# Performance work log

Hardware: AMD Instinct MI355X
Metric: run time of the kernel (lower is better)

The kernel has to match this reference:

```python
import jax, jax.numpy as jnp
import numpy as np

B, D, L = 8, 512, 2000          # batch, encoder_out_dim, seq_len
E = 300                          # embedding_dim
N1, N2 = 118, 8929               # hierarchy level sizes


def setup_inputs() -> dict:
    key = jax.random.key(0)
    k = jax.random.split(key, 6)
    H = jax.random.normal(k[0], (B, D, L), dtype=jnp.float32)
    Q1w = jax.random.normal(k[1], (N1, E), dtype=jnp.float32) * 0.05   # cat_embedding_matrix
    Q2w = jax.random.normal(k[2], (N2, E), dtype=jnp.float32) * 0.05   # label_embedding_matrix
    # Q12: xavier_uniform over [N2, N1]
    bound = float(np.sqrt(6.0 / (N1 + N2)))
    Q12w = jax.random.uniform(k[3], (N2, N1), minval=-bound, maxval=bound, dtype=jnp.float32)
    # 1x1 conv mapping: weight [D, E], bias [D] (kernel_size=1 squeezed)
    cbound = float(np.sqrt(1.0 / E))
    Wmap = jax.random.uniform(k[4], (D, E), minval=-cbound, maxval=cbound, dtype=jnp.float32)
    bmap = jax.random.uniform(k[5], (D,), minval=-cbound, maxval=cbound, dtype=jnp.float32)
    return {"H": H, "Q1w": Q1w, "Q2w": Q2w, "Q12w": Q12w, "Wmap": Wmap, "bmap": bmap}


def reference(H, Q1w, Q2w, Q12w, Wmap, bmap):
    # 1x1 conv mapping == affine map over embedding dim: [n, E] @ [E, D] + b
    Q1 = Q1w @ Wmap.T + bmap                      # [N1, D]
    E1 = jnp.einsum('nd,bdl->bnl', Q1, H)         # level-1 scores [B, N1, L]
    A1 = jax.nn.softmax(E1, axis=2)
    C1 = jnp.einsum('bnl,bdl->bnd', A1, H)        # [B, N1, D]
    C1 = jnp.einsum('mn,bnd->bmd', Q12w, C1)      # project to level 2: [B, N2, D]
    Q2 = (Q2w @ Wmap.T + bmap) * C1               # [N2, D] * [B, N2, D]
    E2 = jnp.einsum('bmd,bdl->bml', Q2, H)        # level-2 scores [B, N2, L]
    A2 = jax.nn.softmax(E2, axis=2)
    C2 = jnp.einsum('bml,bdl->bmd', A2, H)        # [B, N2, D]
    return (C2, A2)
```

## Files before the change

kernel.cpp:

```cpp
#include <hip/hip_runtime.h>

typedef short    bf16x8 __attribute__((ext_vector_type(8)));
typedef float    f32x4  __attribute__((ext_vector_type(4)));
typedef unsigned short u16x8 __attribute__((ext_vector_type(8)));

__device__ __forceinline__ unsigned short f2bf(float f) {
    unsigned u = __float_as_uint(f);
    return (unsigned short)((u + 0x7fffu + ((u >> 16) & 1u)) >> 16);
}
__device__ __forceinline__ float bf2f(unsigned short h) {
    return __uint_as_float((unsigned)h << 16);
}

template<bool> struct otype            { using T = float; };
template<>     struct otype<true>      { using T = unsigned short; };

template<int BM,int BN,int TM,int TN,bool BT,bool VA,bool VB,bool OB>
__launch_bounds__(256)
__global__ void gemm_f32(const float* __restrict__ A, int lda, long long sA,
                         const float* __restrict__ B, int ldb, long long sB,
                         void* __restrict__ Cv, int ldc, long long sC,
                         int M, int N, int K,
                         const float* __restrict__ bias,
                         const float* __restrict__ mul, int mulld)
{
    constexpr int BK  = 16;
    constexpr int GSA = BM*4/TM;
    constexpr int GSB = BN*4/TN;
    __shared__ float As[BK][BM+4];
    __shared__ float Bs[BK][BN+4];

    const int bz = blockIdx.z;
    A += (long long)bz * sA;
    B += (long long)bz * sB;
    using OT = typename otype<OB>::T;
    OT* C = (OT*)Cv + (long long)bz * sC;
    const int m0 = blockIdx.y * BM;
    const int n0 = blockIdx.x * BN;
    const int tid = threadIdx.x;
    const int tm = tid >> 4;
    const int tn = tid & 15;

    float acc[TM][TN];
#pragma unroll
    for (int i=0;i<TM;++i)
#pragma unroll
        for (int j=0;j<TN;++j) acc[i][j]=0.f;

    for (int k0=0;k0<K;k0+=BK) {
        if constexpr (VA) {
#pragma unroll
            for (int r=0;r<BM*BK/1024;++r) {
                int v = tid + r*256;
                int m = v >> 2, k4 = (v & 3)*4;
                int gm = m0+m, gk = k0+k4;
                float4 val = make_float4(0.f,0.f,0.f,0.f);
                if (gm < M) {
                    if (gk+3 < K) {
                        val = *reinterpret_cast<const float4*>(A + (long long)gm*lda + gk);
                    } else {
                        float t0 = (gk   < K) ? A[(long long)gm*lda+gk  ] : 0.f;
                        float t1 = (gk+1 < K) ? A[(long long)gm*lda+gk+1] : 0.f;
                        float t2 = (gk+2 < K) ? A[(long long)gm*lda+gk+2] : 0.f;
                        val = make_float4(t0,t1,t2,0.f);
                    }
                }
                As[k4+0][m]=val.x; As[k4+1][m]=val.y; As[k4+2][m]=val.z; As[k4+3][m]=val.w;
            }
        } else {
#pragma unroll
            for (int r=0;r<BM*BK/256;++r) {
                int e = tid + r*256;
                int m = e >> 4, k = e & 15;
                int gm=m0+m, gk=k0+k;
                As[k][m] = (gm<M && gk<K) ? A[(long long)gm*lda+gk] : 0.f;
            }
        }
        if constexpr (!BT) {
            if constexpr (VB) {
#pragma unroll
                for (int r=0;r<BK*BN/1024;++r) {
                    int v = tid + r*256;
                    int k = v / (BN/4), n4 = (v % (BN/4))*4;
                    int gk=k0+k, gn=n0+n4;
                    float4 val = make_float4(0.f,0.f,0.f,0.f);
                    if (gk < K) {
                        if (gn+3 < N) {
                            val = *reinterpret_cast<const float4*>(B + (long long)gk*ldb + gn);
                        } else {
                            float t0=(gn  <N)?B[(long long)gk*ldb+gn  ]:0.f;
                            float t1=(gn+1<N)?B[(long long)gk*ldb+gn+1]:0.f;
                            float t2=(gn+2<N)?B[(long long)gk*ldb+gn+2]:0.f;
                            val = make_float4(t0,t1,t2,0.f);
                        }
                    }
                    Bs[k][n4+0]=val.x; Bs[k][n4+1]=val.y; Bs[k][n4+2]=val.z; Bs[k][n4+3]=val.w;
                }
            } else {
#pragma unroll
                for (int r=0;r<BK*BN/256;++r) {
                    int e = tid + r*256;
                    int k = e / BN, n = e % BN;
                    int gk=k0+k, gn=n0+n;
                    Bs[k][n] = (gk<K && gn<N) ? B[(long long)gk*ldb+gn] : 0.f;
                }
            }
        } else {
            if constexpr (VB) {
#pragma unroll
                for (int r=0;r<BN*BK/1024;++r) {
                    int v = tid + r*256;
                    int n = v >> 2, k4 = (v&3)*4;
                    int gn=n0+n, gk=k0+k4;
                    float4 val = make_float4(0.f,0.f,0.f,0.f);
                    if (gn < N) {
                        if (gk+3 < K) {
                            val = *reinterpret_cast<const float4*>(B + (long long)gn*ldb + gk);
                        } else {
                            float t0=(gk  <K)?B[(long long)gn*ldb+gk  ]:0.f;
                            float t1=(gk+1<K)?B[(long long)gn*ldb+gk+1]:0.f;
                            float t2=(gk+2<K)?B[(long long)gn*ldb+gk+2]:0.f;
                            val=make_float4(t0,t1,t2,0.f);
                        }
                    }
                    Bs[k4+0][n]=val.x; Bs[k4+1][n]=val.y; Bs[k4+2][n]=val.z; Bs[k4+3][n]=val.w;
                }
            } else {
#pragma unroll
                for (int r=0;r<BN*BK/256;++r) {
                    int e = tid + r*256;
                    int n = e >> 4, k = e & 15;
                    int gn=n0+n, gk=k0+k;
                    Bs[k][n] = (gn<N && gk<K) ? B[(long long)gn*ldb+gk] : 0.f;
                }
            }
        }
        __syncthreads();
#pragma unroll
        for (int kk=0;kk<BK;++kk) {
            float a[TM], bb[TN];
#pragma unroll
            for (int g=0;g<TM/4;++g) {
                float4 t = *reinterpret_cast<const float4*>(&As[kk][g*GSA + tm*4]);
                a[4*g+0]=t.x; a[4*g+1]=t.y; a[4*g+2]=t.z; a[4*g+3]=t.w;
            }
#pragma unroll
            for (int g=0;g<TN/4;++g) {
                float4 t = *reinterpret_cast<const float4*>(&Bs[kk][g*GSB + tn*4]);
                bb[4*g+0]=t.x; bb[4*g+1]=t.y; bb[4*g+2]=t.z; bb[4*g+3]=t.w;
            }
#pragma unroll
            for (int i=0;i<TM;++i)
#pragma unroll
                for (int j=0;j<TN;++j)
                    acc[i][j] = fmaf(a[i], bb[j], acc[i][j]);
        }
        __syncthreads();
    }
#pragma unroll
    for (int i=0;i<TM;++i) {
        int row = m0 + (i>>2)*GSA + tm*4 + (i&3);
        if (row < M) {
#pragma unroll
            for (int j=0;j<TN;++j) {
                int col = n0 + (j>>2)*GSB + tn*4 + (j&3);
                if (col < N) {
                    float val = acc[i][j];
                    if (bias) val += bias[col];
                    if (mul)  val *= mul[(long long)row*mulld + col];
                    if constexpr (OB) C[(long long)row*ldc + col] = f2bf(val);
                    else              C[(long long)row*ldc + col] = val;
                }
            }
        }
    }
}

template<unsigned F>
__launch_bounds__(512, 4)
__global__ void gemm_mfma_p(const unsigned short* __restrict__ A, int lda, long long sA,
                            const unsigned short* __restrict__ Bt, int ldb, long long sB,
                            void* __restrict__ Cv, int ldc, long long sC,
                            int M, int Ncols, int NX, int NY, int NT,
                            const float* __restrict__ bias,
                            const float* __restrict__ mul, int ldm,
                            float* __restrict__ partial, long long pstride,
                            const float* __restrict__ hsum,
                            const float* __restrict__ invs,
                            float* __restrict__ a2out,
                            float* __restrict__ dump)
{
    __shared__ unsigned short lds[3][12288];

    const int nwg = gridDim.x;
    const int q = nwg >> 3, r = nwg & 7;
    const int xcd = blockIdx.x & 7, idx = blockIdx.x >> 3;
    const int wg = (xcd < r ? xcd*(q+1) : r*(q+1) + (xcd-r)*q) + idx;
    const int nx = wg % NX;
    const int t1 = wg / NX;
    const int my = t1 % NY;
    const int bz = t1 / NY;

    const int tid  = threadIdx.x;
    const int lane = tid & 63, wid = tid >> 6;
    const int wr = wid >> 2, wc = wid & 3;
    const int fr = lane & 15, fq = lane >> 4;
    const int m0 = my * 128;
    const int n0 = nx * 256;

    A  += (long long)bz * sA;
    Bt += (long long)bz * sB;

    const int srow = tid >> 2;
    const int scz  = (tid & 3) ^ ((srow >> 1) & 3);
    long long arow = m0 + srow; if (arow > M-1) arow = M-1;
    const unsigned short* aSrc  = A  + arow*lda + scz*8;
    const unsigned short* bSrc0 = Bt + (long long)(n0 + srow)*ldb + scz*8;
    const unsigned short* bSrc1 = bSrc0 + 128ll*ldb;

    bool wrblk = false, a2ok = false;
    float invv = 0.f;
    float* a2p = nullptr;
    if constexpr ((F & 64) != 0) {
        wrblk = (nx == 0);
        if (wrblk) {
            const int rrow = m0 + srow;
            a2ok = rrow < M;
            const long long ridx = (long long)bz*M + (a2ok ? rrow : M-1);
            invv = invs[ridx];
            asm volatile("" : "+v"(invv));
            a2p = a2out + ridx*2000ll;
        }
    }

    int aoff[4], boff[4];
#pragma unroll
    for (int m=0;m<4;++m) {
        const int ra = wr*64 + m*16 + fr;
        aoff[m] = ra*64 + ((fq ^ ((ra>>1)&3))*16);
    }
#pragma unroll
    for (int n=0;n<4;++n) {
        const int rb = wc*64 + n*16 + fr;
        boff[n] = 8192 + rb*64 + ((fq ^ ((rb>>1)&3))*16);
    }

    f32x4 acc[4][4];
#pragma unroll
    for (int i=0;i<4;++i)
#pragma unroll
        for (int j=0;j<4;++j) acc[i][j] = (f32x4)(0.f);

    auto stage = [&](int s, int t) {
        const int koff = t*32;
        char* base = (char*)&lds[s][0];
        __builtin_amdgcn_global_load_lds(
            (const __attribute__((address_space(1))) void*)(aSrc + koff),
            (__attribute__((address_space(3))) void*)(base + tid*16), 16, 0, 0);
        __builtin_amdgcn_global_load_lds(
            (const __attribute__((address_space(1))) void*)(bSrc0 + koff),
            (__attribute__((address_space(3))) void*)(base + 8192 + tid*16), 16, 0, 0);
        __builtin_amdgcn_global_load_lds(
            (const __attribute__((address_space(1))) void*)(bSrc1 + koff),
            (__attribute__((address_space(3))) void*)(base + 16384 + tid*16), 16, 0, 0);
    };

    stage(0, 0);
    stage(1, NT > 1 ? 1 : 0);
    asm volatile("s_waitcnt vmcnt(3)" ::: "memory");
    __builtin_amdgcn_s_barrier();

    int cur = 0, stg = 2;
    for (int kt = 0; kt < NT; ++kt) {
        int tnx = kt + 2; if (tnx > NT-1) tnx = NT-1;
        stage(stg, tnx);
        const char* bp = (const char*)&lds[cur][0];
        bf16x8 a[4], b[4];
#pragma unroll
        for (int m=0;m<4;++m) a[m] = *(const bf16x8*)(bp + aoff[m]);
#pragma unroll
        for (int n=0;n<4;++n) b[n] = *(const bf16x8*)(bp + boff[n]);
        __builtin_amdgcn_s_setprio(1);
#pragma unroll
        for (int m=0;m<4;++m)
#pragma unroll
            for (int n=0;n<4;++n)
                acc[m][n] = __builtin_amdgcn_mfma_f32_16x16x32_bf16(a[m], b[n], acc[m][n], 0, 0, 0);
        __builtin_amdgcn_s_setprio(0);
        if constexpr ((F & 64) != 0) {
            if (wrblk) {
                u16x8 av = *(const u16x8*)(bp + (tid << 4));
                const int col0 = kt*32 + scz*8;
                const bool ok = a2ok && (col0 < 2000);
                float* p0 = ok ? (a2p + col0) : (dump + (tid << 3));
                float4 o0, o1;
                o0.x = fmaf(bf2f((unsigned short)av[0]), invv, invv);
                o0.y = fmaf(bf2f((unsigned short)av[1]), invv, invv);
                o0.z = fmaf(bf2f((unsigned short)av[2]), invv, invv);
                o0.w = fmaf(bf2f((unsigned short)av[3]), invv, invv);
                o1.x = fmaf(bf2f((unsigned short)av[4]), invv, invv);
                o1.y = fmaf(bf2f((unsigned short)av[5]), invv, invv);
                o1.z = fmaf(bf2f((unsigned short)av[6]), invv, invv);
                o1.w = fmaf(bf2f((unsigned short)av[7]), invv, invv);
                *(float4*)(p0    ) = o0;
                *(float4*)(p0 + 4) = o1;
            }
        }
        asm volatile("s_waitcnt lgkmcnt(0)" ::: "memory");
        if constexpr ((F & 64) != 0) {
            if (wrblk) asm volatile("s_waitcnt vmcnt(5)" ::: "memory");
            else       asm volatile("s_waitcnt vmcnt(3)" ::: "memory");
        } else {
            asm volatile("s_waitcnt vmcnt(3)" ::: "memory");
        }
        __builtin_amdgcn_s_barrier();
        cur = (cur == 2) ? 0 : cur + 1;
        stg = (stg == 2) ? 0 : stg + 1;
    }

    if constexpr ((F & 16) != 0) {
        __shared__ float sp[4][128];
        unsigned short* Cb = (unsigned short*)Cv + (long long)bz * sC;
        float rp[4][4];
#pragma unroll
        for (int m=0;m<4;++m)
#pragma unroll
            for (int j=0;j<4;++j) rp[m][j] = 0.f;
#pragma unroll
        for (int m=0;m<4;++m) {
            const int rb = m0 + wr*64 + m*16 + fq*4;
#pragma unroll
            for (int n=0;n<4;++n) {
                const int col = n0 + wc*64 + n*16 + fr;
#pragma unroll
                for (int j=0;j<4;++j) {
                    float x = __expf(acc[m][n][j]) - 1.0f;
                    rp[m][j] += x;
                    const int row = rb + j;
                    if (row < M) Cb[(long long)row*ldc + col] = f2bf(x);
                }
            }
        }
#pragma unroll
        for (int m=0;m<4;++m)
#pragma unroll
            for (int j=0;j<4;++j) {
                float s = rp[m][j];
                s += __shfl_xor(s, 1); s += __shfl_xor(s, 2);
                s += __shfl_xor(s, 4); s += __shfl_xor(s, 8);
                rp[m][j] = s;
            }
        if (fr == 0) {
#pragma unroll
            for (int m=0;m<4;++m)
#pragma unroll
                for (int j=0;j<4;++j)
                    sp[wc][wr*64 + m*16 + fq*4 + j] = rp[m][j];
        }
        __syncthreads();
        if (tid < 128) {
            const int row = m0 + tid;
            if (row < M) {
                float s = sp[0][tid] + sp[1][tid] + sp[2][tid] + sp[3][tid];
                partial[(long long)nx*pstride + (long long)bz*M + row] = s;
            }
        }
    } else if constexpr ((F & 8) != 0) {
        unsigned short* Ct = (unsigned short*)Cv + (long long)bz * sC;
#pragma unroll
        for (int m=0;m<4;++m) {
            const int rb = m0 + wr*64 + m*16 + fq*4;
#pragma unroll
            for (int n=0;n<4;++n) {
                const int col = n0 + wc*64 + n*16 + fr;
                if (col < Ncols) {
#pragma unroll
                    for (int j=0;j<4;++j) {
                        const int row = rb + j;
                        float val = (row < M) ? acc[m][n][j] : 0.f;
                        Ct[(long long)col*ldc + row] = f2bf(val);
                    }
                }
            }
        }
    } else {
        float*          Cf = (float*)Cv + (long long)bz * sC;
        unsigned short* Cb = (unsigned short*)Cv + (long long)bz * sC;
#pragma unroll
        for (int m=0;m<4;++m) {
            const int rb = m0 + wr*64 + m*16 + fq*4;
#pragma unroll
            for (int n=0;n<4;++n) {
                const int col = n0 + wc*64 + n*16 + fr;
                if (col < Ncols) {
                    float bv = 0.f, hv = 0.f;
                    if constexpr ((F & 1) != 0) bv = bias[col];
                    if constexpr ((F & 32) != 0) hv = hsum[(long long)bz*Ncols + col];
#pragma unroll
                    for (int j=0;j<4;++j) {
                        const int row = rb + j;
                        if (row < M) {
                            float val = acc[m][n][j];
                            if constexpr ((F & 1) != 0)  val += bv;
                            if constexpr ((F & 2) != 0)  val *= mul[(long long)row*ldm + col];
                            if constexpr ((F & 32) != 0) val = (val + hv) * invs[(long long)bz*M + row];
                            if constexpr ((F & 4) != 0)  Cb[(long long)row*ldc + col] = f2bf(val);
                            else                         Cf[(long long)row*ldc + col] = val;
                        }
                    }
                }
            }
        }
    }
}

template<bool AF32>
__launch_bounds__(512, 2)
__global__ void gemm_mfma(const void* __restrict__ Ain, int lda, long long sA,
                          const unsigned short* __restrict__ Bt, int ldb, long long sB,
                          float* __restrict__ C, int ldc, long long sC,
                          int M, int N, int K, int NT)
{
    __shared__ unsigned short As[2][128*32];
    __shared__ unsigned short Bs[2][256*32];

    const int tid  = threadIdx.x;
    const int lane = tid & 63, wid = tid >> 6;
    const int wr = wid >> 2, wc = wid & 3;
    const int fr = lane & 15, fq = lane >> 4;
    const int bz = blockIdx.z;
    const int m0 = blockIdx.y * 128;
    const int n0 = blockIdx.x * 256;

    const unsigned short* Ab = nullptr;
    const float*          Af = nullptr;
    if constexpr (AF32) Af = (const float*)Ain + (long long)bz * sA;
    else                Ab = (const unsigned short*)Ain + (long long)bz * sA;
    Bt += (long long)bz * sB;
    C  += (long long)bz * sC;

    const int srow = tid >> 2;
    const int sc   = tid & 3;
    const int scz  = sc ^ ((srow >> 1) & 3);
    int arow = m0 + srow; if (arow > M-1) arow = M-1;
    const bool am_ok = (m0 + srow) < M;
    const long long brow0 = n0 + srow;
    const long long brow1 = n0 + 128 + srow;
    const int ldsA  = wid << 10;
    const int ldsB0 = wid << 10;
    const int ldsB1 = 8192 + (wid << 10);

    f32x4 acc[4][4];
#pragma unroll
    for (int i=0;i<4;++i)
#pragma unroll
        for (int j=0;j<4;++j) acc[i][j] = (f32x4)(0.f);

    auto stage = [&](int buf, int t) {
        const long long koff = (long long)t * 32;
        __builtin_amdgcn_global_load_lds(
            (const __attribute__((address_space(1))) void*)(Bt + brow0*ldb + koff + scz*8),
            (__attribute__((address_space(3))) void*)((char*)&Bs[buf][0] + ldsB0), 16, 0, 0);
        __builtin_amdgcn_global_load_lds(
            (const __attribute__((address_space(1))) void*)(Bt + brow1*ldb + koff + scz*8),
            (__attribute__((address_space(3))) void*)((char*)&Bs[buf][0] + ldsB1), 16, 0, 0);
        if constexpr (!AF32) {
            __builtin_amdgcn_global_load_lds(
                (const __attribute__((address_space(1))) void*)(Ab + (long long)arow*lda + koff + scz*8),
                (__attribute__((address_space(3))) void*)((char*)&As[buf][0] + ldsA), 16, 0, 0);
        } else {
            const float* src = Af + (long long)arow*lda + koff + scz*8;
            const int kk = t*32 + scz*8;
            float4 z = make_float4(0.f,0.f,0.f,0.f);
            float4 v0 = (am_ok && kk   < K) ? *(const float4*)(src  ) : z;
            float4 v1 = (am_ok && kk+4 < K) ? *(const float4*)(src+4) : z;
            u16x8 o;
            o[0]=f2bf(v0.x); o[1]=f2bf(v0.y); o[2]=f2bf(v0.z); o[3]=f2bf(v0.w);
            o[4]=f2bf(v1.x); o[5]=f2bf(v1.y); o[6]=f2bf(v1.z); o[7]=f2bf(v1.w);
            *(u16x8*)((char*)&As[buf][0] + tid*16) = o;
        }
    };

    stage(0, 0);
    int cur = 0;
    for (int t = 0; t < NT; ++t) {
        __syncthreads();
        if (t + 1 < NT) stage(cur ^ 1, t + 1);
        const unsigned short* as = As[cur];
        const unsigned short* bs = Bs[cur];
        bf16x8 a[4], b[4];
#pragma unroll
        for (int m=0;m<4;++m) {
            const int ra = wr*64 + m*16 + fr;
            a[m] = *(const bf16x8*)(as + ra*32 + (fq ^ ((ra>>1)&3))*8);
        }
#pragma unroll
        for (int n=0;n<4;++n) {
            const int rb = wc*64 + n*16 + fr;
            b[n] = *(const bf16x8*)(bs + rb*32 + (fq ^ ((rb>>1)&3))*8);
        }
        __builtin_amdgcn_s_setprio(1);
#pragma unroll
        for (int m=0;m<4;++m)
#pragma unroll
            for (int n=0;n<4;++n)
                acc[m][n] = __builtin_amdgcn_mfma_f32_16x16x32_bf16(a[m], b[n], acc[m][n], 0, 0, 0);
        __builtin_amdgcn_s_setprio(0);
        cur ^= 1;
    }
#pragma unroll
    for (int m=0;m<4;++m) {
        const int rb = m0 + wr*64 + m*16 + fq*4;
#pragma unroll
        for (int n=0;n<4;++n) {
            const int col = n0 + wc*64 + n*16 + fr;
            if (col < N) {
#pragma unroll
                for (int j=0;j<4;++j) {
                    const int row = rb + j;
                    if (row < M) C[(long long)row*ldc + col] = acc[m][n][j];
                }
            }
        }
    }
}

__global__ __launch_bounds__(256) void prep_h(const float* __restrict__ H,
                                              unsigned short* __restrict__ Hb,
                                              unsigned short* __restrict__ Htb,
                                              float* __restrict__ hpart)
{
    __shared__ unsigned short T[64][80];
    const int bz = blockIdx.z;
    const int d0 = blockIdx.y * 64;
    const int l0 = blockIdx.x * 64;
    const float* Hsrc = H + ((long long)bz*512 + d0) * 2000;
    const int tid = threadIdx.x;
    const int dl = tid >> 2;
    const int lc = (tid & 3) * 16;
    float4 v[4];
    float s = 0.f;
#pragma unroll
    for (int i=0;i<4;++i) {
        const int gl = l0 + lc + i*4;
        v[i] = make_float4(0.f,0.f,0.f,0.f);
        if (gl < 2000) v[i] = *(const float4*)(Hsrc + (long long)dl*2000 + gl);
        s += (v[i].x + v[i].y) + (v[i].z + v[i].w);
        T[lc+i*4+0][dl] = f2bf(v[i].x);
        T[lc+i*4+1][dl] = f2bf(v[i].y);
        T[lc+i*4+2][dl] = f2bf(v[i].z);
        T[lc+i*4+3][dl] = f2bf(v[i].w);
    }
    {
        unsigned short* hb = Hb + ((long long)bz*512 + d0 + dl)*2048 + l0 + lc;
        u16x8 h0, h1;
        h0[0]=f2bf(v[0].x); h0[1]=f2bf(v[0].y); h0[2]=f2bf(v[0].z); h0[3]=f2bf(v[0].w);
        h0[4]=f2bf(v[1].x); h0[5]=f2bf(v[1].y); h0[6]=f2bf(v[1].z); h0[7]=f2bf(v[1].w);
        h1[0]=f2bf(v[2].x); h1[1]=f2bf(v[2].y); h1[2]=f2bf(v[2].z); h1[3]=f2bf(v[2].w);
        h1[4]=f2bf(v[3].x); h1[5]=f2bf(v[3].y); h1[6]=f2bf(v[3].z); h1[7]=f2bf(v[3].w);
        *(u16x8*)(hb    ) = h0;
        *(u16x8*)(hb + 8) = h1;
    }
    s += __shfl_xor(s, 1);
    s += __shfl_xor(s, 2);
    if ((tid & 3) == 0)
        hpart[(long long)blockIdx.x*4096 + bz*512 + d0 + dl] = s;
    __syncthreads();
    unsigned short* Hdst = Htb + ((long long)bz*2048 + l0) * 512 + d0;
    const int ll = tid >> 2;
    const int dc = (tid & 3) * 16;
    u16x8 w0 = *(const u16x8*)&T[ll][dc];
    u16x8 w1 = *(const u16x8*)&T[ll][dc+8];
    *(u16x8*)(Hdst + (long long)ll*512 + dc    ) = w0;
    *(u16x8*)(Hdst + (long long)ll*512 + dc + 8) = w1;
}

__global__ __launch_bounds__(256) void reduce_hsum(const float* __restrict__ hpart,
                                                   float* __restrict__ Hsum)
{
    const int r = blockIdx.x*256 + threadIdx.x;
    float s = 0.f;
#pragma unroll
    for (int i=0;i<32;++i) s += hpart[(long long)i*4096 + r];
    Hsum[r] = s;
}

__global__ __launch_bounds__(256) void invs_k(const float* __restrict__ partial,
                                              long long pstride,
                                              float* __restrict__ invs, int n)
{
    const int r = blockIdx.x*256 + threadIdx.x;
    if (r < n) {
        float s = 0.f;
#pragma unroll
        for (int i=0;i<8;++i) s += partial[i*pstride + r];
        invs[r] = 1.0f / (2000.0f + s);
    }
}

__global__ __launch_bounds__(256) void cvt_pad_bf16(const float* __restrict__ H,
                                                    unsigned short* __restrict__ Hb)
{
    const long long idx = (long long)blockIdx.x * 256 + threadIdx.x;
    const long long row = idx >> 8;
    const int l0 = (int)(idx & 255) * 8;
    u16x8 o = (u16x8)(unsigned short)0;
    if (l0 + 8 <= 2000) {
        const float* s = H + row*2000 + l0;
        float4 v0 = *(const float4*)(s);
        float4 v1 = *(const float4*)(s+4);
        o[0]=f2bf(v0.x); o[1]=f2bf(v0.y); o[2]=f2bf(v0.z); o[3]=f2bf(v0.w);
        o[4]=f2bf(v1.x); o[5]=f2bf(v1.y); o[6]=f2bf(v1.z); o[7]=f2bf(v1.w);
    }
    *(u16x8*)(Hb + row*2048 + l0) = o;
}

__global__ __launch_bounds__(256) void cvt_transpose_bf16(const float* __restrict__ H,
                                                          unsigned short* __restrict__ Ht)
{
    __shared__ unsigned short T[64][80];
    const int bz = blockIdx.z;
    const int d0 = blockIdx.y * 64;
    const int l0 = blockIdx.x * 64;
    const float* Hsrc = H + ((long long)bz*512 + d0) * 2000;
    unsigned short* Hdst = Ht + ((long long)bz*2048 + l0) * 512 + d0;
    const int tid = threadIdx.x;
    const int dl = tid >> 2;
    const int lc = (tid & 3) * 16;
#pragma unroll
    for (int i=0;i<4;++i) {
        const int l = lc + i*4;
        const int gl = l0 + l;
        float4 v = make_float4(0.f,0.f,0.f,0.f);
        if (gl < 2000) v = *(const float4*)(Hsrc + (long long)dl*2000 + gl);
        T[l+0][dl] = f2bf(v.x);
        T[l+1][dl] = f2bf(v.y);
        T[l+2][dl] = f2bf(v.z);
        T[l+3][dl] = f2bf(v.w);
    }
    __syncthreads();
    const int ll = tid >> 2;
    const int dc = (tid & 3) * 16;
    u16x8 w0 = *(const u16x8*)&T[ll][dc];
    u16x8 w1 = *(const u16x8*)&T[ll][dc+8];
    *(u16x8*)(Hdst + (long long)ll*512 + dc    ) = w0;
    *(u16x8*)(Hdst + (long long)ll*512 + dc + 8) = w1;
}

__global__ __launch_bounds__(256) void cvt_rows_bf16(const float* __restrict__ src,
                                                     unsigned short* __restrict__ dst,
                                                     long long rows, int scols, int dcols)
{
    const long long i = (long long)blockIdx.x * 256 + threadIdx.x;
    if (i < rows * (long long)dcols) {
        const long long r = i / dcols;
        const int c = (int)(i - r*dcols);
        dst[i] = (c < scols) ? f2bf(src[r*scols + c]) : (unsigned short)0;
    }
}

__global__ __launch_bounds__(256) void softmax_rows(float* __restrict__ X, int L,
                                                    unsigned short* __restrict__ Xb, int Lb)
{
    const long long row = blockIdx.x;
    float* x = X + row * (long long)L;
    const int tid = threadIdx.x;
    const int nv = L >> 2;
    const bool h0 = tid < nv;
    const bool h1 = tid + 256 < nv;
    float4 t0 = make_float4(0.f,0.f,0.f,0.f);
    float4 t1 = make_float4(0.f,0.f,0.f,0.f);
    float mx = -3.402823e38f;
    if (h0) { t0 = *reinterpret_cast<const float4*>(x + 4*tid);
              mx = fmaxf(fmaxf(t0.x,t0.y), fmaxf(t0.z,t0.w)); }
    if (h1) { t1 = *reinterpret_cast<const float4*>(x + 4*(tid+256));
              mx = fmaxf(mx, fmaxf(fmaxf(t1.x,t1.y), fmaxf(t1.z,t1.w))); }
    __shared__ float sred[4];
#pragma unroll
    for (int o=32;o;o>>=1) mx = fmaxf(mx, __shfl_xor(mx, o));
    if ((tid & 63)==0) sred[tid>>6] = mx;
    __syncthreads();
    mx = fmaxf(fmaxf(sred[0],sred[1]), fmaxf(sred[2],sred[3]));
    __syncthreads();
    float s = 0.f;
    if (h0) {
        t0.x=__expf(t0.x-mx); t0.y=__expf(t0.y-mx); t0.z=__expf(t0.z-mx); t0.w=__expf(t0.w-mx);
        s += (t0.x+t0.y)+(t0.z+t0.w);
    }
    if (h1) {
        t1.x=__expf(t1.x-mx); t1.y=__expf(t1.y-mx); t1.z=__expf(t1.z-mx); t1.w=__expf(t1.w-mx);
        s += (t1.x+t1.y)+(t1.z+t1.w);
    }
#pragma unroll
    for (int o=32;o;o>>=1) s += __shfl_xor(s, o);
    if ((tid & 63)==0) sred[tid>>6] = s;
    __syncthreads();
    s = (sred[0]+sred[1])+(sred[2]+sred[3]);
    const float inv = 1.0f / s;
    if (h0) { t0.x*=inv; t0.y*=inv; t0.z*=inv; t0.w*=inv;
              *reinterpret_cast<float4*>(x + 4*tid) = t0; }
    if (h1) { t1.x*=inv; t1.y*=inv; t1.z*=inv; t1.w*=inv;
              *reinterpret_cast<float4*>(x + 4*(tid+256)) = t1; }
    if (Xb) {
        unsigned short* xb = Xb + row * (long long)Lb;
        if (h0) {
            ushort4 o; o.x=f2bf(t0.x); o.y=f2bf(t0.y); o.z=f2bf(t0.z); o.w=f2bf(t0.w);
            *reinterpret_cast<ushort4*>(xb + 4*tid) = o;
        }
        if (h1) {
            ushort4 o; o.x=f2bf(t1.x); o.y=f2bf(t1.y); o.z=f2bf(t1.z); o.w=f2bf(t1.w);
            *reinterpret_cast<ushort4*>(xb + 4*(tid+256)) = o;
        }
        if (tid < (Lb - L)/4) {
            ushort4 z; z.x=z.y=z.z=z.w=0;
            *reinterpret_cast<ushort4*>(xb + L + 4*tid) = z;
        }
    }
}

extern "C" void kernel_launch(void* const* d_in, const int* in_sizes, int n_in,
                              void* d_out, int out_size, void* d_ws, size_t ws_size,
                              hipStream_t stream)
{
    const float* H    = (const float*)d_in[0];
    const float* Q1w  = (const float*)d_in[1];
    const float* Q2w  = (const float*)d_in[2];
    const float* Q12w = (const float*)d_in[3];
    const float* Wmap = (const float*)d_in[4];
    const float* bmap = (const float*)d_in[5];

    constexpr long long B=8, D=512, L=2000, N1=118, N2=8929;
    constexpr long long C2E = B*N2*D;
    float* out = (float*)d_out;
    float* C2  = out;
    float* A2  = out + C2E;

    dim3 blk(256);

    size_t off = 0;
    auto alloc = [&](size_t n)->size_t { off = (off + 255) & ~(size_t)255; size_t o = off; off += n; return o; };
    const size_t oHb    = alloc(8ll*512*2048*2);
    const size_t oHtb   = alloc(8ll*2048*512*2);
    const size_t oWb    = alloc(512ll*320*2);
    const size_t oQ1wb  = alloc(118ll*320*2);
    const size_t oQ2wb  = alloc(8929ll*320*2);
    const size_t oQ12wb = alloc(8929ll*128*2);
    const size_t oQ1b   = alloc(118ll*512*2);
    const size_t oEmb   = alloc(8929ll*512*4);
    const size_t oE1    = alloc(8ll*118*2000*4);
    const size_t oA1b   = alloc(8ll*118*2048*2);
    const size_t oC1tb  = alloc(8ll*512*128*2);
    const size_t oQ2b   = alloc(8ll*8929*512*2);
    const size_t oA2b   = alloc(8ll*8929*2048*2);
    const size_t oPart  = alloc(8ll*8*8929*4);
    const size_t oInvs  = alloc(8ll*8929*4);
    const size_t oHsum  = alloc(8ll*512*4);
    const size_t oHpart = alloc(32ll*4096*4);
    const size_t FULL_NEED = off;

    char* ws = (char*)d_ws;

    if (ws_size >= FULL_NEED) {
        unsigned short* Hb    = (unsigned short*)(ws + oHb);
        unsigned short* Htb   = (unsigned short*)(ws + oHtb);
        unsigned short* Wb    = (unsigned short*)(ws + oWb);
        unsigned short* Q1wb  = (unsigned short*)(ws + oQ1wb);
        unsigned short* Q2wb  = (unsigned short*)(ws + oQ2wb);
        unsigned short* Q12wb = (unsigned short*)(ws + oQ12wb);
        unsigned short* Q1b   = (unsigned short*)(ws + oQ1b);
        float*          emb   = (float*)(ws + oEmb);
        float*          E1    = (float*)(ws + oE1);
        unsigned short* A1b   = (unsigned short*)(ws + oA1b);
        unsigned short* C1tb  = (unsigned short*)(ws + oC1tb);
        unsigned short* Q2b   = (unsigned short*)(ws + oQ2b);
        unsigned short* A2b   = (unsigned short*)(ws + oA2b);
        float*          part  = (float*)(ws + oPart);
        float*          invs  = (float*)(ws + oInvs);
        float*          Hsum  = (float*)(ws + oHsum);
        float*          hpart = (float*)(ws + oHpart);

        prep_h<<<dim3(32,8,8), blk, 0, stream>>>(H, Hb, Htb, hpart);
        reduce_hsum<<<dim3(16), blk, 0, stream>>>(hpart, Hsum);
        cvt_rows_bf16<<<dim3((512*320+255)/256), blk, 0, stream>>>(Wmap, Wb, 512, 300, 320);
        cvt_rows_bf16<<<dim3((118*320+255)/256), blk, 0, stream>>>(Q1w, Q1wb, 118, 300, 320);
        cvt_rows_bf16<<<dim3((8929*320+255)/256), blk, 0, stream>>>(Q2w, Q2wb, 8929, 300, 320);
        cvt_rows_bf16<<<dim3((8929*128+255)/256), blk, 0, stream>>>(Q12w, Q12wb, 8929, 118, 128);

        gemm_mfma_p<5><<<dim3(2), dim3(512), 0, stream>>>(
            Q1wb, 320, 0, Wb, 320, 0, Q1b, 512, 0, 118, 512, 2, 1, 10,
            bmap, nullptr, 0, nullptr, 0, nullptr, nullptr, nullptr, nullptr);
        gemm_mfma_p<1><<<dim3(140), dim3(512), 0, stream>>>(
            Q2wb, 320, 0, Wb, 320, 0, emb, 512, 0, 8929, 512, 2, 70, 10,
            bmap, nullptr, 0, nullptr, 0, nullptr, nullptr, nullptr, nullptr);
        gemm_mfma_p<0><<<dim3(64), dim3(512), 0, stream>>>(
            Q1b, 512, 0, Htb, 512, 2048*512, E1, 2000, N1*L, 118, 2000, 8, 1, 16,
            nullptr, nullptr, 0, nullptr, 0, nullptr, nullptr, nullptr, nullptr);
        softmax_rows<<<dim3((unsigned)(B*N1)), blk, 0, stream>>>(E1, 2000, A1b, 2048);
        gemm_mfma_p<12><<<dim3(16), dim3(512), 0, stream>>>(
            A1b, 2048, N1*2048, Hb, 2048, 512*2048, C1tb, 128, 512*128, 118, 512, 2, 1, 64,
            nullptr, nullptr, 0, nullptr, 0, nullptr, nullptr, nullptr, nullptr);
        gemm_mfma_p<6><<<dim3(1120), dim3(512), 0, stream>>>(
            Q12wb, 128, 0, C1tb, 128, 512*128, Q2b, 512, N2*D, 8929, 512, 2, 70, 4,
            nullptr, emb, 512, nullptr, 0, nullptr, nullptr, nullptr, nullptr);
        gemm_mfma_p<16><<<dim3(4480), dim3(512), 0, stream>>>(
            Q2b, 512, N2*D, Htb, 512, 2048*512, A2b, 2048, N2*2048, 8929, 2048, 8, 70, 16,
            nullptr, nullptr, 0, part, 8ll*8929, nullptr, nullptr, nullptr, nullptr);
        invs_k<<<dim3(280), blk, 0, stream>>>(part, 8ll*8929, invs, (int)(B*N2));
        gemm_mfma_p<96><<<dim3(1120), dim3(512), 0, stream>>>(
            A2b, 2048, N2*2048, Hb, 2048, 512*2048, C2, 512, N2*D, 8929, 512, 2, 70, 64,
            nullptr, nullptr, 0, nullptr, 0, Hsum, invs, A2, part);
        return;
    }

    float* Q1  = A2;
    float* emb = Q1  + N1*D;
    float* E1  = emb + N2*D;
    float* C1  = E1  + B*N1*L;

    gemm_f32<64,64,4,4,true,true,true,false><<<dim3(8,2,1), blk, 0, stream>>>(
        Q1w, 300, 0, Wmap, 300, 0, Q1, 512, 0, (int)N1, (int)D, 300, bmap, nullptr, 0);
    gemm_f32<64,64,4,4,true,true,true,false><<<dim3(8,140,1), blk, 0, stream>>>(
        Q2w, 300, 0, Wmap, 300, 0, emb, 512, 0, (int)N2, (int)D, 300, bmap, nullptr, 0);
    gemm_f32<64,64,4,4,false,true,true,false><<<dim3(32,2,8), blk, 0, stream>>>(
        Q1, 512, 0, H, 2000, D*L, E1, 2000, N1*L, (int)N1, (int)L, (int)D, nullptr, nullptr, 0);
    softmax_rows<<<dim3((unsigned)(B*N1)), blk, 0, stream>>>(E1, (int)L, nullptr, 0);
    gemm_f32<64,64,4,4,true,true,true,false><<<dim3(8,2,8), blk, 0, stream>>>(
        E1, 2000, N1*L, H, 2000, D*L, C1, 512, N1*D, (int)N1, (int)D, (int)L, nullptr, nullptr, 0);

    constexpr long long HBE = 8ll*512*2048;
    if (ws_size >= (size_t)(2*HBE*sizeof(unsigned short))) {
        unsigned short* Hb  = (unsigned short*)d_ws;
        unsigned short* Htb = Hb + HBE;
        cvt_pad_bf16<<<dim3(4096), blk, 0, stream>>>(H, Hb);
        cvt_transpose_bf16<<<dim3(32,8,8), blk, 0, stream>>>(H, Htb);
        unsigned short* Q2b = (unsigned short*)C2;
        gemm_f32<64,64,4,4,false,false,true,true><<<dim3(8,140,8), blk, 0, stream>>>(
            Q12w, 118, 0, C1, 512, N1*D, Q2b, 512, N2*D, (int)N2, (int)D, (int)N1, nullptr, emb, 512);
        gemm_mfma_p<0><<<dim3(4480), dim3(512), 0, stream>>>(
            Q2b, 512, N2*D, Htb, 512, 2048*512, A2, 2000, N2*L, (int)N2, (int)L, 8, 70, 16,
            nullptr, nullptr, 0, nullptr, 0, nullptr, nullptr, nullptr, nullptr);
        softmax_rows<<<dim3((unsigned)(B*N2)), blk, 0, stream>>>(A2, (int)L, nullptr, 0);
        gemm_mfma<true><<<dim3(2,70,8), dim3(512), 0, stream>>>(
            A2, 2000, N2*L, Hb, 2048, 512*2048, C2, 512, N2*D,
            (int)N2, (int)D, 2000, 63);
    } else {
        float* Q2 = C2;
        gemm_f32<64,64,4,4,false,false,true,false><<<dim3(8,140,8), blk, 0, stream>>>(
            Q12w, 118, 0, C1, 512, N1*D, Q2, 512, N2*D, (int)N2, (int)D, (int)N1, nullptr, emb, 512);
        gemm_f32<128,128,8,8,false,true,true,false><<<dim3(16,70,8), blk, 0, stream>>>(
            Q2, 512, N2*D, H, 2000, D*L, A2, 2000, N2*L, (int)N2, (int)L, (int)D, nullptr, nullptr, 0);
        softmax_rows<<<dim3((unsigned)(B*N2)), blk, 0, stream>>>(A2, (int)L, nullptr, 0);
        gemm_f32<128,128,8,8,true,true,true,false><<<dim3(4,70,8), blk, 0, stream>>>(
            A2, 2000, N2*L, H, 2000, D*L, C2, 512, N2*D, (int)N2, (int)D, (int)L, nullptr, nullptr, 0);
    }
}
```

Measured before the change: 810.4 us.

## Fuse prep kernels, reuse fused-softmax GEMM path for level 1, split A2 writes

Merges the H transpose/convert kernel and four weight-conversion kernels into one launch. The level-1 path drops the fp32 score buffer and separate softmax: it uses the exp-partial-sum GEMM variant (F=16) plus invs_k, and folds normalization into the C1 GEMM epilogue via Hsum and invs1. The embedding intermediate is stored as bf16 and read through a new F&128 multiply path. The fp32 A2 output writes are spread across both column blocks by alternating k-tiles, instead of being done only by the nx==0 blocks. This cuts launches and memory traffic but adds bf16 rounding on the embedding product.

```diff
diff --git a/kernel.cpp b/kernel.cpp
--- a/kernel.cpp
+++ b/kernel.cpp
@@ -218,19 +218,18 @@
     const unsigned short* bSrc0 = Bt + (long long)(n0 + srow)*ldb + scz*8;
     const unsigned short* bSrc1 = bSrc0 + 128ll*ldb;
 
-    bool wrblk = false, a2ok = false;
+    bool a2ok = false;
+    int  par  = 0;
     float invv = 0.f;
     float* a2p = nullptr;
     if constexpr ((F & 64) != 0) {
-        wrblk = (nx == 0);
-        if (wrblk) {
-            const int rrow = m0 + srow;
-            a2ok = rrow < M;
-            const long long ridx = (long long)bz*M + (a2ok ? rrow : M-1);
-            invv = invs[ridx];
-            asm volatile("" : "+v"(invv));
-            a2p = a2out + ridx*2000ll;
-        }
+        par = nx & 1;
+        const int rrow = m0 + srow;
+        a2ok = rrow < M;
+        const long long ridx = (long long)bz*M + (a2ok ? rrow : M-1);
+        invv = invs[ridx];
+        asm volatile("" : "+v"(invv));
+        a2p = a2out + ridx*2000ll;
     }
 
     int aoff[4], boff[4];
@@ -288,7 +287,7 @@
                 acc[m][n] = __builtin_amdgcn_mfma_f32_16x16x32_bf16(a[m], b[n], acc[m][n], 0, 0, 0);
         __builtin_amdgcn_s_setprio(0);
         if constexpr ((F & 64) != 0) {
-            if (wrblk) {
+            if ((kt & 1) == par) {
                 u16x8 av = *(const u16x8*)(bp + (tid << 4));
                 const int col0 = kt*32 + scz*8;
                 const bool ok = a2ok && (col0 < 2000);
@@ -308,8 +307,7 @@
         }
         asm volatile("s_waitcnt lgkmcnt(0)" ::: "memory");
         if constexpr ((F & 64) != 0) {
-            if (wrblk) asm volatile("s_waitcnt vmcnt(5)" ::: "memory");
-            else       asm volatile("s_waitcnt vmcnt(3)" ::: "memory");
+            asm volatile("s_waitcnt vmcnt(5)" ::: "memory");
         } else {
             asm volatile("s_waitcnt vmcnt(3)" ::: "memory");
         }
@@ -374,10 +372,16 @@
             for (int n=0;n<4;++n) {
                 const int col = n0 + wc*64 + n*16 + fr;
                 if (col < Ncols) {
+                    float hv = 0.f;
+                    if constexpr ((F & 32) != 0) hv = hsum[(long long)bz*Ncols + col];
 #pragma unroll
                     for (int j=0;j<4;++j) {
                         const int row = rb + j;
-                        float val = (row < M) ? acc[m][n][j] : 0.f;
+                        float val = 0.f;
+                        if (row < M) {
+                            val = acc[m][n][j];
+                            if constexpr ((F & 32) != 0) val = (val + hv) * invs[(long long)bz*M + row];
+                        }
                         Ct[(long long)col*ldc + row] = f2bf(val);
                     }
                 }
@@ -401,11 +405,12 @@
                         const int row = rb + j;
                         if (row < M) {
                             float val = acc[m][n][j];
-                            if constexpr ((F & 1) != 0)  val += bv;
-                            if constexpr ((F & 2) != 0)  val *= mul[(long long)row*ldm + col];
-                            if constexpr ((F & 32) != 0) val = (val + hv) * invs[(long long)bz*M + row];
-                            if constexpr ((F & 4) != 0)  Cb[(long long)row*ldc + col] = f2bf(val);
-                            else                         Cf[(long long)row*ldc + col] = val;
+                            if constexpr ((F & 1)   != 0) val += bv;
+                            if constexpr ((F & 2)   != 0) val *= mul[(long long)row*ldm + col];
+                            if constexpr ((F & 128) != 0) val *= bf2f(((const unsigned short*)mul)[(long long)row*ldm + col]);
+                            if constexpr ((F & 32)  != 0) val = (val + hv) * invs[(long long)bz*M + row];
+                            if constexpr ((F & 4)   != 0) Cb[(long long)row*ldc + col] = f2bf(val);
+                            else                          Cf[(long long)row*ldc + col] = val;
                         }
                     }
                 }
@@ -525,54 +530,76 @@
     }
 }
 
-__global__ __launch_bounds__(256) void prep_h(const float* __restrict__ H,
-                                              unsigned short* __restrict__ Hb,
-                                              unsigned short* __restrict__ Htb,
-                                              float* __restrict__ hpart)
+__global__ __launch_bounds__(256) void mega_prep(const float* __restrict__ H,
+                                                 unsigned short* __restrict__ Hb,
+                                                 unsigned short* __restrict__ Htb,
+                                                 float* __restrict__ hpart,
+                                                 const float* __restrict__ Wmap,  unsigned short* __restrict__ Wb,
+                                                 const float* __restrict__ Q1w,   unsigned short* __restrict__ Q1wb,
+                                                 const float* __restrict__ Q2w,   unsigned short* __restrict__ Q2wb,
+                                                 const float* __restrict__ Q12w,  unsigned short* __restrict__ Q12wb)
 {
     __shared__ unsigned short T[64][80];
-    const int bz = blockIdx.z;
-    const int d0 = blockIdx.y * 64;
-    const int l0 = blockIdx.x * 64;
-    const float* Hsrc = H + ((long long)bz*512 + d0) * 2000;
     const int tid = threadIdx.x;
-    const int dl = tid >> 2;
-    const int lc = (tid & 3) * 16;
-    float4 v[4];
-    float s = 0.f;
-#pragma unroll
-    for (int i=0;i<4;++i) {
-        const int gl = l0 + lc + i*4;
-        v[i] = make_float4(0.f,0.f,0.f,0.f);
-        if (gl < 2000) v[i] = *(const float4*)(Hsrc + (long long)dl*2000 + gl);
-        s += (v[i].x + v[i].y) + (v[i].z + v[i].w);
-        T[lc+i*4+0][dl] = f2bf(v[i].x);
-        T[lc+i*4+1][dl] = f2bf(v[i].y);
-        T[lc+i*4+2][dl] = f2bf(v[i].z);
-        T[lc+i*4+3][dl] = f2bf(v[i].w);
-    }
-    {
-        unsigned short* hb = Hb + ((long long)bz*512 + d0 + dl)*2048 + l0 + lc;
-        u16x8 h0, h1;
-        h0[0]=f2bf(v[0].x); h0[1]=f2bf(v[0].y); h0[2]=f2bf(v[0].z); h0[3]=f2bf(v[0].w);
-        h0[4]=f2bf(v[1].x); h0[5]=f2bf(v[1].y); h0[6]=f2bf(v[1].z); h0[7]=f2bf(v[1].w);
-        h1[0]=f2bf(v[2].x); h1[1]=f2bf(v[2].y); h1[2]=f2bf(v[2].z); h1[3]=f2bf(v[2].w);
-        h1[4]=f2bf(v[3].x); h1[5]=f2bf(v[3].y); h1[6]=f2bf(v[3].z); h1[7]=f2bf(v[3].w);
-        *(u16x8*)(hb    ) = h0;
-        *(u16x8*)(hb + 8) = h1;
-    }
-    s += __shfl_xor(s, 1);
-    s += __shfl_xor(s, 2);
-    if ((tid & 3) == 0)
-        hpart[(long long)blockIdx.x*4096 + bz*512 + d0 + dl] = s;
-    __syncthreads();
-    unsigned short* Hdst = Htb + ((long long)bz*2048 + l0) * 512 + d0;
-    const int ll = tid >> 2;
-    const int dc = (tid & 3) * 16;
-    u16x8 w0 = *(const u16x8*)&T[ll][dc];
-    u16x8 w1 = *(const u16x8*)&T[ll][dc+8];
-    *(u16x8*)(Hdst + (long long)ll*512 + dc    ) = w0;
-    *(u16x8*)(Hdst + (long long)ll*512 + dc + 8) = w1;
+    int id = blockIdx.x;
+    if (id < 2048) {
+        const int lt = id & 31;
+        const int dt = (id >> 5) & 7;
+        const int bz = id >> 8;
+        const int d0 = dt * 64;
+        const int l0 = lt * 64;
+        const float* Hsrc = H + ((long long)bz*512 + d0) * 2000;
+        const int dl = tid >> 2;
+        const int lc = (tid & 3) * 16;
+        float4 v[4];
+        float s = 0.f;
+#pragma unroll
+        for (int i=0;i<4;++i) {
+            const int gl = l0 + lc + i*4;
+            v[i] = make_float4(0.f,0.f,0.f,0.f);
+            if (gl < 2000) v[i] = *(const float4*)(Hsrc + (long long)dl*2000 + gl);
+            s += (v[i].x + v[i].y) + (v[i].z + v[i].w);
+            T[lc+i*4+0][dl] = f2bf(v[i].x);
+            T[lc+i*4+1][dl] = f2bf(v[i].y);
+            T[lc+i*4+2][dl] = f2bf(v[i].z);
+            T[lc+i*4+3][dl] = f2bf(v[i].w);
+        }
+        {
+            unsigned short* hb = Hb + ((long long)bz*512 + d0 + dl)*2048 + l0 + lc;
+            u16x8 h0, h1;
+            h0[0]=f2bf(v[0].x); h0[1]=f2bf(v[0].y); h0[2]=f2bf(v[0].z); h0[3]=f2bf(v[0].w);
+            h0[4]=f2bf(v[1].x); h0[5]=f2bf(v[1].y); h0[6]=f2bf(v[1].z); h0[7]=f2bf(v[1].w);
+            h1[0]=f2bf(v[2].x); h1[1]=f2bf(v[2].y); h1[2]=f2bf(v[2].z); h1[3]=f2bf(v[2].w);
+            h1[4]=f2bf(v[3].x); h1[5]=f2bf(v[3].y); h1[6]=f2bf(v[3].z); h1[7]=f2bf(v[3].w);
+            *(u16x8*)(hb    ) = h0;
+            *(u16x8*)(hb + 8) = h1;
+        }
+        s += __shfl_xor(s, 1);
+        s += __shfl_xor(s, 2);
+        if ((tid & 3) == 0)
+            hpart[(long long)lt*4096 + bz*512 + d0 + dl] = s;
+        __syncthreads();
+        unsigned short* Hdst = Htb + ((long long)bz*2048 + l0) * 512 + d0;
+        const int ll = tid >> 2;
+        const int dc = (tid & 3) * 16;
+        u16x8 w0 = *(const u16x8*)&T[ll][dc];
+        u16x8 w1 = *(const u16x8*)&T[ll][dc+8];
+        *(u16x8*)(Hdst + (long long)ll*512 + dc    ) = w0;
+        *(u16x8*)(Hdst + (long long)ll*512 + dc + 8) = w1;
+        return;
+    }
+    id -= 2048;
+    const float* src; unsigned short* dst; long long tot; int sc, dc;
+    if (id < 640)        { src=Wmap;  dst=Wb;    tot=512ll*320;  sc=300; dc=320; }
+    else if (id < 788)   { id-=640;   src=Q1w;   dst=Q1wb;  tot=118ll*320;  sc=300; dc=320; }
+    else if (id < 11950) { id-=788;   src=Q2w;   dst=Q2wb;  tot=8929ll*320; sc=300; dc=320; }
+    else                 { id-=11950; src=Q12w;  dst=Q12wb; tot=8929ll*128; sc=118; dc=128; }
+    const long long i = (long long)id*256 + tid;
+    if (i < tot) {
+        const long long rr = i / dc;
+        const int c = (int)(i - rr*dc);
+        dst[i] = (c < sc) ? f2bf(src[rr*sc + c]) : (unsigned short)0;
+    }
 }
 
 __global__ __launch_bounds__(256) void reduce_hsum(const float* __restrict__ hpart,
@@ -645,18 +672,6 @@
     u16x8 w1 = *(const u16x8*)&T[ll][dc+8];
     *(u16x8*)(Hdst + (long long)ll*512 + dc    ) = w0;
     *(u16x8*)(Hdst + (long long)ll*512 + dc + 8) = w1;
-}
-
-__global__ __launch_bounds__(256) void cvt_rows_bf16(const float* __restrict__ src,
-                                                     unsigned short* __restrict__ dst,
-                                                     long long rows, int scols, int dcols)
-{
-    const long long i = (long long)blockIdx.x * 256 + threadIdx.x;
-    if (i < rows * (long long)dcols) {
-        const long long r = i / dcols;
-        const int c = (int)(i - r*dcols);
-        dst[i] = (c < scols) ? f2bf(src[r*scols + c]) : (unsigned short)0;
-    }
 }
 
 __global__ __launch_bounds__(256) void softmax_rows(float* __restrict__ X, int L,
@@ -746,14 +761,15 @@
     const size_t oQ2wb  = alloc(8929ll*320*2);
     const size_t oQ12wb = alloc(8929ll*128*2);
     const size_t oQ1b   = alloc(118ll*512*2);
-    const size_t oEmb   = alloc(8929ll*512*4);
-    const size_t oE1    = alloc(8ll*118*2000*4);
-    const size_t oA1b   = alloc(8ll*118*2048*2);
+    const size_t oEmbb  = alloc(8929ll*512*2);
+    const size_t oE1x   = alloc(8ll*128*2048*2);
     const size_t oC1tb  = alloc(8ll*512*128*2);
     const size_t oQ2b   = alloc(8ll*8929*512*2);
     const size_t oA2b   = alloc(8ll*8929*2048*2);
     const size_t oPart  = alloc(8ll*8*8929*4);
+    const size_t oPart1 = alloc(8ll*944*4);
     const size_t oInvs  = alloc(8ll*8929*4);
+    const size_t oInvs1 = alloc(944ll*4);
     const size_t oHsum  = alloc(8ll*512*4);
     const size_t oHpart = alloc(32ll*4096*4);
     const size_t FULL_NEED = off;
@@ -768,40 +784,38 @@
         unsigned short* Q2wb  = (unsigned short*)(ws + oQ2wb);
         unsigned short* Q12wb = (unsigned short*)(ws + oQ12wb);
         unsigned short* Q1b   = (unsigned short*)(ws + oQ1b);
-        float*          emb   = (float*)(ws + oEmb);
-        float*          E1    = (float*)(ws + oE1);
-        unsigned short* A1b   = (unsigned short*)(ws + oA1b);
+        unsigned short* Embb  = (unsigned short*)(ws + oEmbb);
+        unsigned short* E1x   = (unsigned short*)(ws + oE1x);
         unsigned short* C1tb  = (unsigned short*)(ws + oC1tb);
         unsigned short* Q2b   = (unsigned short*)(ws + oQ2b);
         unsigned short* A2b   = (unsigned short*)(ws + oA2b);
         float*          part  = (float*)(ws + oPart);
+        float*          part1 = (float*)(ws + oPart1);
         float*          invs  = (float*)(ws + oInvs);
+        float*          invs1 = (float*)(ws + oInvs1);
         float*          Hsum  = (float*)(ws + oHsum);
         float*          hpart = (float*)(ws + oHpart);
 
-        prep_h<<<dim3(32,8,8), blk, 0, stream>>>(H, Hb, Htb, hpart);
+        mega_prep<<<dim3(18464), blk, 0, stream>>>(H, Hb, Htb, hpart,
+                                                   Wmap, Wb, Q1w, Q1wb, Q2w, Q2wb, Q12w, Q12wb);
         reduce_hsum<<<dim3(16), blk, 0, stream>>>(hpart, Hsum);
-        cvt_rows_bf16<<<dim3((512*320+255)/256), blk, 0, stream>>>(Wmap, Wb, 512, 300, 320);
-        cvt_rows_bf16<<<dim3((118*320+255)/256), blk, 0, stream>>>(Q1w, Q1wb, 118, 300, 320);
-        cvt_rows_bf16<<<dim3((8929*320+255)/256), blk, 0, stream>>>(Q2w, Q2wb, 8929, 300, 320);
-        cvt_rows_bf16<<<dim3((8929*128+255)/256), blk, 0, stream>>>(Q12w, Q12wb, 8929, 118, 128);
 
         gemm_mfma_p<5><<<dim3(2), dim3(512), 0, stream>>>(
             Q1wb, 320, 0, Wb, 320, 0, Q1b, 512, 0, 118, 512, 2, 1, 10,
             bmap, nullptr, 0, nullptr, 0, nullptr, nullptr, nullptr, nullptr);
-        gemm_mfma_p<1><<<dim3(140), dim3(512), 0, stream>>>(
-            Q2wb, 320, 0, Wb, 320, 0, emb, 512, 0, 8929, 512, 2, 70, 10,
+        gemm_mfma_p<5><<<dim3(140), dim3(512), 0, stream>>>(
+            Q2wb, 320, 0, Wb, 320, 0, Embb, 512, 0, 8929, 512, 2, 70, 10,
             bmap, nullptr, 0, nullptr, 0, nullptr, nullptr, nullptr, nullptr);
-        gemm_mfma_p<0><<<dim3(64), dim3(512), 0, stream>>>(
-            Q1b, 512, 0, Htb, 512, 2048*512, E1, 2000, N1*L, 118, 2000, 8, 1, 16,
-            nullptr, nullptr, 0, nullptr, 0, nullptr, nullptr, nullptr, nullptr);
-        softmax_rows<<<dim3((unsigned)(B*N1)), blk, 0, stream>>>(E1, 2000, A1b, 2048);
-        gemm_mfma_p<12><<<dim3(16), dim3(512), 0, stream>>>(
-            A1b, 2048, N1*2048, Hb, 2048, 512*2048, C1tb, 128, 512*128, 118, 512, 2, 1, 64,
-            nullptr, nullptr, 0, nullptr, 0, nullptr, nullptr, nullptr, nullptr);
-        gemm_mfma_p<6><<<dim3(1120), dim3(512), 0, stream>>>(
+        gemm_mfma_p<16><<<dim3(64), dim3(512), 0, stream>>>(
+            Q1b, 512, 0, Htb, 512, 2048*512, E1x, 2048, 128*2048, 118, 2048, 8, 1, 16,
+            nullptr, nullptr, 0, part1, 944, nullptr, nullptr, nullptr, nullptr);
+        invs_k<<<dim3(4), blk, 0, stream>>>(part1, 944, invs1, 944);
+        gemm_mfma_p<40><<<dim3(16), dim3(512), 0, stream>>>(
+            E1x, 2048, 128*2048, Hb, 2048, 512*2048, C1tb, 128, 512*128, 118, 512, 2, 1, 64,
+            nullptr, nullptr, 0, nullptr, 0, Hsum, invs1, nullptr, nullptr);
+        gemm_mfma_p<132><<<dim3(1120), dim3(512), 0, stream>>>(
             Q12wb, 128, 0, C1tb, 128, 512*128, Q2b, 512, N2*D, 8929, 512, 2, 70, 4,
-            nullptr, emb, 512, nullptr, 0, nullptr, nullptr, nullptr, nullptr);
+            nullptr, (const float*)Embb, 512, nullptr, 0, nullptr, nullptr, nullptr, nullptr);
         gemm_mfma_p<16><<<dim3(4480), dim3(512), 0, stream>>>(
             Q2b, 512, N2*D, Htb, 512, 2048*512, A2b, 2048, N2*2048, 8929, 2048, 8, 70, 16,
             nullptr, nullptr, 0, part, 8ll*8929, nullptr, nullptr, nullptr, nullptr);
```

After: 822.9 us. About the same (+1.5%).
